# Kernel optimization log

Hardware: AMD Instinct MI355X
Metric: run time of the kernel (lower is better)

Reference implementation:

```python
import jax, jax.numpy as jnp
import numpy as np

B, G, P, E, H, K = 16, 512, 512, 256, 16, 16
CLIP = 10.0

def setup_inputs() -> dict:
    key = jax.random.key(0)
    ks = jax.random.split(key, 10)
    d = {
        "input1": jax.random.normal(ks[0], (B, 1, E), jnp.float32),
        "input2": jax.random.normal(ks[1], (B, G, E), jnp.float32),
        "current_time": jax.random.uniform(ks[2], (B, G, 1), jnp.float32),
        "ninf_mask": jnp.zeros((B, G, P), jnp.float32),
        "encoded_nodes": jax.random.normal(ks[3], (B, P, E), jnp.float32),
        # learned params (Linear weights stored [in, out]; y = x @ W)
        "Wq": jax.random.normal(ks[4], (2 * E + 1, H * K), jnp.float32) / np.sqrt(2 * E + 1),
        "Wk": jax.random.normal(ks[5], (E, H * K), jnp.float32) / np.sqrt(E),
        "Wv": jax.random.normal(ks[6], (E, H * K), jnp.float32) / np.sqrt(E),
        "Wc_w": jax.random.normal(ks[7], (H * K, E), jnp.float32) / np.sqrt(H * K),
        "Wc_b": jax.random.normal(ks[8], (E,), jnp.float32) * 0.01,
    }
    return d

def _heads(x):  # [B, N, H*K] -> [B, H, N, K]
    b, n, _ = x.shape
    return x.reshape(b, n, H, K).transpose(0, 2, 1, 3)

def reference(input1, input2, current_time, ninf_mask, encoded_nodes, Wq, Wk, Wv, Wc_w, Wc_b):
    # reset(): precompute k, v, single_head_key from encoded_nodes
    k = _heads(encoded_nodes @ Wk)  # [B,H,P,K]
    v = _heads(encoded_nodes @ Wv)  # [B,H,P,K]

    # forward()
    input_cat = jnp.concatenate(
        (jnp.broadcast_to(input1, (B, G, E)), input2, current_time), axis=2)  # [B,G,2E+1]
    q = _heads(input_cat @ Wq)  # [B,H,G,K]

    # MHA with additive ninf mask
    score = jnp.einsum("bhgk,bhpk->bhgp", q, k) / np.sqrt(K)
    score = score + ninf_mask[:, None, :, :]
    weights = jax.nn.softmax(score, axis=3)
    out = jnp.einsum("bhgp,bhpk->bhgk", weights, v)
    out_concat = out.transpose(0, 2, 1, 3).reshape(B, G, H * K)
    mh_atten_out = out_concat @ Wc_w + Wc_b  # [B,G,E]

    # single-head pointer score with tanh clipping
    score2 = jnp.einsum("bge,bpe->bgp", mh_atten_out, encoded_nodes) / np.sqrt(E)
    score_clipped = CLIP * jnp.tanh(score2)
    probs = jax.nn.softmax(score_clipped + ninf_mask, axis=2)
    return probs
```

## Files before the change

kernel.cpp:

```cpp
#include <hip/hip_runtime.h>
#include <math.h>

#define BB 16
#define GG 512
#define PP 512
#define EE 256
#define HH 16
#define KD 16
#define HK 256

typedef __bf16 bf16x8 __attribute__((ext_vector_type(8)));
typedef __bf16 bf16x4 __attribute__((ext_vector_type(4)));
typedef float f32x4 __attribute__((ext_vector_type(4)));
typedef float f32x16 __attribute__((ext_vector_type(16)));

#define SA_STRIDE 40
#define SMEM_BYTES 30720

__device__ inline void cvt_split8(const float* __restrict__ p, bf16x8& h, bf16x8& l)
{
    float4 f0 = *(const float4*)p;
    float4 f1 = *(const float4*)(p + 4);
    float v[8] = {f0.x, f0.y, f0.z, f0.w, f1.x, f1.y, f1.z, f1.w};
#pragma unroll
    for (int j = 0; j < 8; ++j) {
        __bf16 hh = (__bf16)v[j];
        h[j] = hh;
        l[j] = (__bf16)(v[j] - (float)hh);
    }
}

__global__ __launch_bounds__(256) void weight_prep(const float* __restrict__ Wk,
                                                   const float* __restrict__ Wv,
                                                   const float* __restrict__ Wq,
                                                   const float* __restrict__ Wc,
                                                   __bf16* __restrict__ wkt_h, __bf16* __restrict__ wkt_l,
                                                   __bf16* __restrict__ wvt_h, __bf16* __restrict__ wvt_l,
                                                   __bf16* __restrict__ wqt_h, __bf16* __restrict__ wqt_l,
                                                   __bf16* __restrict__ wct_h, __bf16* __restrict__ wct_l)
{
    int id = blockIdx.x * 256 + threadIdx.x;
    const float* W;
    __bf16 *th, *tl;
    int kbits;
    if (id < 65536)       { W = Wk; th = wkt_h; tl = wkt_l; kbits = 8; }
    else if (id < 131072) { id -= 65536;  W = Wv; th = wvt_h; tl = wvt_l; kbits = 8; }
    else if (id < 262144) { id -= 131072; W = Wq; th = wqt_h; tl = wqt_l; kbits = 9; }
    else                  { id -= 262144; W = Wc; th = wct_h; tl = wct_l; kbits = 8; }
    const int Kd = 1 << kbits;
    const int k = id & (Kd - 1);
    const int n = id >> kbits;
    const float v = W[(size_t)k * HK + n];
    const __bf16 h = (__bf16)v;
    th[((size_t)n << kbits) + k] = h;
    tl[((size_t)n << kbits) + k] = (__bf16)(v - (float)h);
}

__device__ inline void kvproj_body(int bx, int tid, unsigned char* smem,
                                   const float* __restrict__ A,
                                   const __bf16* __restrict__ Bkh,
                                   const __bf16* __restrict__ Bkl,
                                   const __bf16* __restrict__ Bvh,
                                   const __bf16* __restrict__ Bvl,
                                   __bf16* __restrict__ Khi,
                                   __bf16* __restrict__ Klo,
                                   __bf16* __restrict__ Vt)
{
    __bf16* sAh = (__bf16*)smem;
    __bf16* sAl = sAh + 64 * SA_STRIDE;
    __bf16* sB  = sAl + 64 * SA_STRIDE;

    const int lane = tid & 63;
    const int w = __builtin_amdgcn_readfirstlane(tid >> 6);
    const int m0 = (bx >> 2) * 64;
    const int n0 = (bx & 3) * 64;
    const int wm = (w >> 1) * 32, wn = (w & 1) * 32;
    const int ln = lane & 15, kq = (lane >> 4) * 8;
    const int ar = tid >> 2, ac = (tid & 3) * 8;

    const __bf16* bsel = (w == 0) ? Bkh : (w == 1) ? Bkl : (w == 2) ? Bvh : Bvl;

    f32x4 ak[2][2], av[2][2];
#pragma unroll
    for (int i = 0; i < 2; ++i)
#pragma unroll
        for (int j = 0; j < 2; ++j) {
            ak[i][j] = (f32x4){0.f, 0.f, 0.f, 0.f};
            av[i][j] = (f32x4){0.f, 0.f, 0.f, 0.f};
        }

    for (int k0 = 0; k0 < EE; k0 += 32) {
        {
            bf16x8 h8, l8;
            cvt_split8(A + (size_t)(m0 + ar) * EE + k0 + ac, h8, l8);
            *(bf16x8*)&sAh[ar * SA_STRIDE + ac] = h8;
            *(bf16x8*)&sAl[ar * SA_STRIDE + ac] = l8;
        }
        {
            const __bf16* src = bsel + (size_t)(n0 + lane) * EE + k0;
            __bf16* dst = sB + (w * 64 + lane) * SA_STRIDE;
            *(bf16x8*)&dst[0]  = *(const bf16x8*)&src[0];
            *(bf16x8*)&dst[8]  = *(const bf16x8*)&src[8];
            *(bf16x8*)&dst[16] = *(const bf16x8*)&src[16];
            *(bf16x8*)&dst[24] = *(const bf16x8*)&src[24];
        }
        __syncthreads();

        bf16x8 ah[2], al[2];
#pragma unroll
        for (int mt = 0; mt < 2; ++mt) {
            ah[mt] = *(const bf16x8*)&sAh[(wm + mt * 16 + ln) * SA_STRIDE + kq];
            al[mt] = *(const bf16x8*)&sAl[(wm + mt * 16 + ln) * SA_STRIDE + kq];
        }
#pragma unroll
        for (int nt = 0; nt < 2; ++nt) {
            const int rowb = wn + nt * 16 + ln;
            bf16x8 bkh8 = *(const bf16x8*)&sB[(0 * 64 + rowb) * SA_STRIDE + kq];
            bf16x8 bkl8 = *(const bf16x8*)&sB[(1 * 64 + rowb) * SA_STRIDE + kq];
            bf16x8 bvh8 = *(const bf16x8*)&sB[(2 * 64 + rowb) * SA_STRIDE + kq];
            bf16x8 bvl8 = *(const bf16x8*)&sB[(3 * 64 + rowb) * SA_STRIDE + kq];
#pragma unroll
            for (int mt = 0; mt < 2; ++mt) {
                ak[mt][nt] = __builtin_amdgcn_mfma_f32_16x16x32_bf16(ah[mt], bkh8, ak[mt][nt], 0, 0, 0);
                ak[mt][nt] = __builtin_amdgcn_mfma_f32_16x16x32_bf16(al[mt], bkh8, ak[mt][nt], 0, 0, 0);
                ak[mt][nt] = __builtin_amdgcn_mfma_f32_16x16x32_bf16(ah[mt], bkl8, ak[mt][nt], 0, 0, 0);
                av[mt][nt] = __builtin_amdgcn_mfma_f32_16x16x32_bf16(ah[mt], bvh8, av[mt][nt], 0, 0, 0);
                av[mt][nt] = __builtin_amdgcn_mfma_f32_16x16x32_bf16(al[mt], bvh8, av[mt][nt], 0, 0, 0);
                av[mt][nt] = __builtin_amdgcn_mfma_f32_16x16x32_bf16(ah[mt], bvl8, av[mt][nt], 0, 0, 0);
            }
        }
        __syncthreads();
    }

    __bf16* eKh = (__bf16*)smem;
    __bf16* eKl = eKh + 5120;
    __bf16* eV  = eKl + 5120;

    const int rbase = (lane >> 4) * 4;
#pragma unroll
    for (int mt = 0; mt < 2; ++mt)
#pragma unroll
        for (int nt = 0; nt < 2; ++nt) {
            const int hloc = (w & 1) * 2 + nt;
            const int nl = wn + nt * 16 + ln;
#pragma unroll
            for (int r = 0; r < 4; ++r) {
                const int m = wm + mt * 16 + rbase + r;
                const float vk = ak[mt][nt][r];
                const __bf16 hk = (__bf16)vk;
                eKh[(hloc * 64 + m) * 20 + ln] = hk;
                eKl[(hloc * 64 + m) * 20 + ln] = (__bf16)(vk - (float)hk);
                eV[nl * 68 + m] = (__bf16)av[mt][nt][r];
            }
        }
    __syncthreads();

    const int b = m0 >> 9;
    const int pbase = m0 & (PP - 1);
    {
        const int hl = tid >> 6, p = tid & 63;
        const int hg = (n0 >> 4) + hl;
        const size_t dst = (((size_t)b * HH + hg) * PP + pbase + p) * KD;
        const int base = (hl * 64 + p) * 20;
        uint2 a0 = *(const uint2*)&eKh[base + 0];
        uint2 a1 = *(const uint2*)&eKh[base + 4];
        uint2 a2 = *(const uint2*)&eKh[base + 8];
        uint2 a3 = *(const uint2*)&eKh[base + 12];
        *(uint4*)(Khi + dst)     = make_uint4(a0.x, a0.y, a1.x, a1.y);
        *(uint4*)(Khi + dst + 8) = make_uint4(a2.x, a2.y, a3.x, a3.y);
        uint2 c0 = *(const uint2*)&eKl[base + 0];
        uint2 c1 = *(const uint2*)&eKl[base + 4];
        uint2 c2 = *(const uint2*)&eKl[base + 8];
        uint2 c3 = *(const uint2*)&eKl[base + 12];
        *(uint4*)(Klo + dst)     = make_uint4(c0.x, c0.y, c1.x, c1.y);
        *(uint4*)(Klo + dst + 8) = make_uint4(c2.x, c2.y, c3.x, c3.y);
    }
    {
        const int n = tid >> 2, qq = tid & 3;
        const int ng = n0 + n, hg = ng >> 4, kk = ng & 15;
        const int base = n * 68 + qq * 16;
        uint2 v0 = *(const uint2*)&eV[base + 0];
        uint2 v1 = *(const uint2*)&eV[base + 4];
        uint2 v2 = *(const uint2*)&eV[base + 8];
        uint2 v3 = *(const uint2*)&eV[base + 12];
        const size_t dst = ((((size_t)b * HH + hg) * KD + kk) * PP) + pbase + qq * 16;
        *(uint4*)(Vt + dst)     = make_uint4(v0.x, v0.y, v1.x, v1.y);
        *(uint4*)(Vt + dst + 8) = make_uint4(v2.x, v2.y, v3.x, v3.y);
    }
}

__device__ inline void qproj_body(int bx, int tid, unsigned char* smem,
                                  const float* __restrict__ in1,
                                  const float* __restrict__ in2,
                                  const float* __restrict__ ct,
                                  const __bf16* __restrict__ Bh,
                                  const __bf16* __restrict__ Bl,
                                  const float* __restrict__ WqFull,
                                  __bf16* __restrict__ Qhi,
                                  __bf16* __restrict__ Qlo)
{
    __bf16* sAh = (__bf16*)smem;
    __bf16* sAl = sAh + 64 * SA_STRIDE;
    __bf16* sB  = sAl + 64 * SA_STRIDE;

    const int lane = tid & 63;
    const int w = __builtin_amdgcn_readfirstlane(tid >> 6);
    const int m0 = (bx >> 2) * 64;
    const int n0 = (bx & 3) * 64;
    const int wm = (w >> 1) * 32, wn = (w & 1) * 32;
    const int ln = lane & 15, kq = (lane >> 4) * 8;
    const int ar = tid >> 2, ac = (tid & 3) * 8;
    const int b = m0 >> 9;
    const float* WqLast = WqFull + (size_t)512 * HK;

    f32x4 acc[2][2];
#pragma unroll
    for (int i = 0; i < 2; ++i)
#pragma unroll
        for (int j = 0; j < 2; ++j) acc[i][j] = (f32x4){0.f, 0.f, 0.f, 0.f};

    for (int k0 = 0; k0 < 512; k0 += 32) {
        {
            const float* ap = (k0 < 256)
                ? in1 + (size_t)b * EE + k0 + ac
                : in2 + (size_t)(m0 + ar) * EE + (k0 - 256) + ac;
            bf16x8 h8, l8;
            cvt_split8(ap, h8, l8);
            *(bf16x8*)&sAh[ar * SA_STRIDE + ac] = h8;
            *(bf16x8*)&sAl[ar * SA_STRIDE + ac] = l8;
        }
        {
            const int mat = w >> 1;
            const int row = (w & 1) * 32 + (lane >> 1);
            const int half = (lane & 1) * 16;
            const __bf16* src = (mat ? Bl : Bh) + ((size_t)(n0 + row) << 9) + k0 + half;
            __bf16* dst = sB + (mat * 64 + row) * SA_STRIDE + half;
            *(bf16x8*)&dst[0] = *(const bf16x8*)&src[0];
            *(bf16x8*)&dst[8] = *(const bf16x8*)&src[8];
        }
        __syncthreads();

        bf16x8 ah[2], al[2];
#pragma unroll
        for (int mt = 0; mt < 2; ++mt) {
            ah[mt] = *(const bf16x8*)&sAh[(wm + mt * 16 + ln) * SA_STRIDE + kq];
            al[mt] = *(const bf16x8*)&sAl[(wm + mt * 16 + ln) * SA_STRIDE + kq];
        }
#pragma unroll
        for (int nt = 0; nt < 2; ++nt) {
            const int rowb = wn + nt * 16 + ln;
            bf16x8 bh8 = *(const bf16x8*)&sB[(0 * 64 + rowb) * SA_STRIDE + kq];
            bf16x8 bl8 = *(const bf16x8*)&sB[(1 * 64 + rowb) * SA_STRIDE + kq];
#pragma unroll
            for (int mt = 0; mt < 2; ++mt) {
                acc[mt][nt] = __builtin_amdgcn_mfma_f32_16x16x32_bf16(ah[mt], bh8, acc[mt][nt], 0, 0, 0);
                acc[mt][nt] = __builtin_amdgcn_mfma_f32_16x16x32_bf16(al[mt], bh8, acc[mt][nt], 0, 0, 0);
                acc[mt][nt] = __builtin_amdgcn_mfma_f32_16x16x32_bf16(ah[mt], bl8, acc[mt][nt], 0, 0, 0);
            }
        }
        __syncthreads();
    }

    __bf16* eQh = (__bf16*)smem;
    __bf16* eQl = eQh + 5120;

    const int rbase = (lane >> 4) * 4;
#pragma unroll
    for (int mt = 0; mt < 2; ++mt)
#pragma unroll
        for (int nt = 0; nt < 2; ++nt) {
            const int hloc = (w & 1) * 2 + nt;
            const int ng = n0 + wn + nt * 16 + ln;
            const float wq = WqLast[ng];
#pragma unroll
            for (int r = 0; r < 4; ++r) {
                const int m = wm + mt * 16 + rbase + r;
                const float v = acc[mt][nt][r] + ct[m0 + m] * wq;
                const __bf16 h = (__bf16)v;
                eQh[(hloc * 64 + m) * 20 + ln] = h;
                eQl[(hloc * 64 + m) * 20 + ln] = (__bf16)(v - (float)h);
            }
        }
    __syncthreads();

    {
        const int hl = tid >> 6, p = tid & 63;
        const int hg = (n0 >> 4) + hl;
        const int g = (m0 & (GG - 1)) + p;
        const size_t dst = (((size_t)b * HH + hg) * GG + g) * KD;
        const int base = (hl * 64 + p) * 20;
        uint2 a0 = *(const uint2*)&eQh[base + 0];
        uint2 a1 = *(const uint2*)&eQh[base + 4];
        uint2 a2 = *(const uint2*)&eQh[base + 8];
        uint2 a3 = *(const uint2*)&eQh[base + 12];
        *(uint4*)(Qhi + dst)     = make_uint4(a0.x, a0.y, a1.x, a1.y);
        *(uint4*)(Qhi + dst + 8) = make_uint4(a2.x, a2.y, a3.x, a3.y);
        uint2 c0 = *(const uint2*)&eQl[base + 0];
        uint2 c1 = *(const uint2*)&eQl[base + 4];
        uint2 c2 = *(const uint2*)&eQl[base + 8];
        uint2 c3 = *(const uint2*)&eQl[base + 12];
        *(uint4*)(Qlo + dst)     = make_uint4(c0.x, c0.y, c1.x, c1.y);
        *(uint4*)(Qlo + dst + 8) = make_uint4(c2.x, c2.y, c3.x, c3.y);
    }
}

__global__ __launch_bounds__(256, 2) void fused_proj(const float* __restrict__ enc,
                                                     const __bf16* __restrict__ Bkh,
                                                     const __bf16* __restrict__ Bkl,
                                                     const __bf16* __restrict__ Bvh,
                                                     const __bf16* __restrict__ Bvl,
                                                     __bf16* __restrict__ Khi,
                                                     __bf16* __restrict__ Klo,
                                                     __bf16* __restrict__ Vt,
                                                     const float* __restrict__ in1,
                                                     const float* __restrict__ in2,
                                                     const float* __restrict__ ct,
                                                     const __bf16* __restrict__ Bqh,
                                                     const __bf16* __restrict__ Bql,
                                                     const float* __restrict__ WqFull,
                                                     __bf16* __restrict__ Qhi,
                                                     __bf16* __restrict__ Qlo)
{
    __shared__ __align__(16) unsigned char smem[SMEM_BYTES];
    const int id = blockIdx.x;
    if (id < 512)
        kvproj_body(id, threadIdx.x, smem, enc, Bkh, Bkl, Bvh, Bvl, Khi, Klo, Vt);
    else
        qproj_body(id - 512, threadIdx.x, smem, in1, in2, ct, Bqh, Bql, WqFull, Qhi, Qlo);
}

__global__ __launch_bounds__(256, 4) void attn_v8(const __bf16* __restrict__ Qhi,
                                                  const __bf16* __restrict__ Qlo,
                                                  const __bf16* __restrict__ Khi,
                                                  const __bf16* __restrict__ Klo,
                                                  const __bf16* __restrict__ Vt,
                                                  const float* __restrict__ mask,
                                                  __bf16* __restrict__ Ath,
                                                  __bf16* __restrict__ Atl)
{
    __shared__ __align__(16) __bf16 sP[4][32][40];
    __shared__ float srs[4][32];

    const int t = threadIdx.x;
    const int lane = t & 63;
    const int w = __builtin_amdgcn_readfirstlane(t >> 6);
    const int g0 = blockIdx.x * 32;
    const int h = blockIdx.y * 4 + w;
    const int b = blockIdx.z;
    const int ln32 = lane & 31;
    const int half = lane >> 5;
    const int ln16 = lane & 15;
    const int quad = (lane >> 4) & 3;

    const size_t qbase = (((size_t)b * HH + h) * GG + g0) * KD;
    const size_t kbase = ((size_t)b * HH + h) * PP * KD;
    const size_t vbase = ((size_t)b * HH + h) * KD * PP;
    const float* mbase = mask + ((size_t)(b * GG + g0)) * PP;

    bf16x8 qah = *(const bf16x8*)(Qhi + qbase + (size_t)ln32 * KD + half * 8);
    bf16x8 qal = *(const bf16x8*)(Qlo + qbase + (size_t)ln32 * KD + half * 8);

    float rs[16];
#pragma unroll
    for (int r = 0; r < 16; ++r) rs[r] = 0.f;
    f32x4 o0 = (f32x4){0.f, 0.f, 0.f, 0.f};
    f32x4 o1 = (f32x4){0.f, 0.f, 0.f, 0.f};

#pragma unroll 2
    for (int pc = 0; pc < 16; ++pc) {
        const int pb = pc * 32;
        const size_t ko = kbase + (size_t)(pb + ln32) * KD + half * 8;
        bf16x8 kh = *(const bf16x8*)(Khi + ko);
        bf16x8 kl = *(const bf16x8*)(Klo + ko);

        f32x16 s = (f32x16){0.f, 0.f, 0.f, 0.f, 0.f, 0.f, 0.f, 0.f,
                            0.f, 0.f, 0.f, 0.f, 0.f, 0.f, 0.f, 0.f};
        s = __builtin_amdgcn_mfma_f32_32x32x16_bf16(qah, kh, s, 0, 0, 0);
        s = __builtin_amdgcn_mfma_f32_32x32x16_bf16(qal, kh, s, 0, 0, 0);
        s = __builtin_amdgcn_mfma_f32_32x32x16_bf16(qah, kl, s, 0, 0, 0);

#pragma unroll
        for (int r = 0; r < 16; ++r) {
            const int row = (r & 3) + 8 * (r >> 2) + 4 * half;
            const float m = mbase[(size_t)row * PP + pb + ln32];
            const float e = __expf(s[r] * 0.25f + m);
            rs[r] += e;
            sP[w][row][ln32] = (__bf16)e;
        }

        bf16x8 vb = *(const bf16x8*)(Vt + vbase + (size_t)ln16 * PP + pb + quad * 8);
        bf16x8 p0 = *(const bf16x8*)&sP[w][ln16][quad * 8];
        bf16x8 p1 = *(const bf16x8*)&sP[w][16 + ln16][quad * 8];
        o0 = __builtin_amdgcn_mfma_f32_16x16x32_bf16(p0, vb, o0, 0, 0, 0);
        o1 = __builtin_amdgcn_mfma_f32_16x16x32_bf16(p1, vb, o1, 0, 0, 0);
    }

#pragma unroll
    for (int r = 0; r < 16; ++r) {
#pragma unroll
        for (int mm = 1; mm < 32; mm <<= 1) rs[r] += __shfl_xor(rs[r], mm);
    }
    if (ln32 == 0) {
#pragma unroll
        for (int r = 0; r < 16; ++r)
            srs[w][(r & 3) + 8 * (r >> 2) + 4 * half] = rs[r];
    }

#pragma unroll
    for (int t2 = 0; t2 < 2; ++t2) {
        const f32x4 oc = t2 ? o1 : o0;
#pragma unroll
        for (int r = 0; r < 4; ++r) {
            const int grow = t2 * 16 + quad * 4 + r;
            const float v = oc[r] / srs[w][grow];
            const __bf16 hv = (__bf16)v;
            const size_t oo = ((size_t)(b * GG + g0 + grow)) * HK + h * KD + ln16;
            Ath[oo] = hv;
            Atl[oo] = (__bf16)(v - (float)hv);
        }
    }
}

__device__ inline void outproj_body(int bx, int tid,
                                    const __bf16* __restrict__ Ah,
                                    const __bf16* __restrict__ Al,
                                    const __bf16* __restrict__ Bh,
                                    const __bf16* __restrict__ Bl,
                                    const float* __restrict__ bias,
                                    __bf16* __restrict__ Ch,
                                    __bf16* __restrict__ Cl)
{
    const int lane = tid & 63, w = tid >> 6;
    const int m0 = (bx >> 2) * 64 + (w >> 1) * 32;
    const int n0 = (bx & 3) * 64 + (w & 1) * 32;
    const int ln = lane & 15, kc = (lane >> 4) * 8;

    f32x4 acc[2][2];
#pragma unroll
    for (int i = 0; i < 2; ++i)
#pragma unroll
        for (int j = 0; j < 2; ++j) acc[i][j] = (f32x4){0.f, 0.f, 0.f, 0.f};

    for (int k0 = 0; k0 < EE; k0 += 32) {
        bf16x8 ah[2], al[2], bh[2], bl[2];
#pragma unroll
        for (int mt = 0; mt < 2; ++mt) {
            const size_t o = (size_t)(m0 + mt * 16 + ln) * EE + k0 + kc;
            ah[mt] = *(const bf16x8*)(Ah + o);
            al[mt] = *(const bf16x8*)(Al + o);
        }
#pragma unroll
        for (int nt = 0; nt < 2; ++nt) {
            const size_t o = (size_t)(n0 + nt * 16 + ln) * EE + k0 + kc;
            bh[nt] = *(const bf16x8*)(Bh + o);
            bl[nt] = *(const bf16x8*)(Bl + o);
        }
#pragma unroll
        for (int mt = 0; mt < 2; ++mt)
#pragma unroll
            for (int nt = 0; nt < 2; ++nt) {
                acc[mt][nt] = __builtin_amdgcn_mfma_f32_16x16x32_bf16(ah[mt], bh[nt], acc[mt][nt], 0, 0, 0);
                acc[mt][nt] = __builtin_amdgcn_mfma_f32_16x16x32_bf16(al[mt], bh[nt], acc[mt][nt], 0, 0, 0);
                acc[mt][nt] = __builtin_amdgcn_mfma_f32_16x16x32_bf16(ah[mt], bl[nt], acc[mt][nt], 0, 0, 0);
            }
    }

    const int rbase = (lane >> 4) * 4;
#pragma unroll
    for (int mt = 0; mt < 2; ++mt)
#pragma unroll
        for (int nt = 0; nt < 2; ++nt)
#pragma unroll
            for (int r = 0; r < 4; ++r) {
                const int m = m0 + rbase + r + mt * 16;
                const int n = n0 + nt * 16 + ln;
                const float v = acc[mt][nt][r] + bias[n];
                const __bf16 h = (__bf16)v;
                Ch[(size_t)m * HK + n] = h;
                Cl[(size_t)m * HK + n] = (__bf16)(v - (float)h);
            }
}

__global__ __launch_bounds__(256) void fused_post(const __bf16* __restrict__ Ah,
                                                  const __bf16* __restrict__ Al,
                                                  const __bf16* __restrict__ Bh,
                                                  const __bf16* __restrict__ Bl,
                                                  const float* __restrict__ bias,
                                                  __bf16* __restrict__ Ch,
                                                  __bf16* __restrict__ Cl,
                                                  const float* __restrict__ enc,
                                                  __bf16* __restrict__ enc_h,
                                                  __bf16* __restrict__ enc_l)
{
    const int id = blockIdx.x;
    if (id < 512) {
        outproj_body(id, threadIdx.x, Ah, Al, Bh, Bl, bias, Ch, Cl);
    } else {
        const int i = ((id - 512) * 256 + threadIdx.x) * 4;
        float4 v = *(const float4*)(enc + i);
        bf16x4 h, l;
        h[0] = (__bf16)v.x; l[0] = (__bf16)(v.x - (float)h[0]);
        h[1] = (__bf16)v.y; l[1] = (__bf16)(v.y - (float)h[1]);
        h[2] = (__bf16)v.z; l[2] = (__bf16)(v.z - (float)h[2]);
        h[3] = (__bf16)v.w; l[3] = (__bf16)(v.w - (float)h[3]);
        *(bf16x4*)(enc_h + i) = h;
        *(bf16x4*)(enc_l + i) = l;
    }
}

__global__ __launch_bounds__(512) void pointer_v3(const __bf16* __restrict__ mh_hi,
                                                  const __bf16* __restrict__ mh_lo,
                                                  const __bf16* __restrict__ enc_hi,
                                                  const __bf16* __restrict__ enc_lo,
                                                  const float* __restrict__ mask,
                                                  float* __restrict__ out)
{
    __shared__ float swsum[8][32];
    const int t = threadIdx.x;
    const int lane = t & 63;
    const int w = __builtin_amdgcn_readfirstlane(t >> 6);
    const int id = blockIdx.x;
    const int b = id & 15;
    const int g0 = (id >> 4) * 32;
    const int ln32 = lane & 31;
    const int half = lane >> 5;

    const size_t arow = ((size_t)(b * GG + g0 + ln32)) * EE + half * 8;
    const size_t brow = ((size_t)(b * PP + w * 64 + ln32)) * EE + half * 8;

    f32x16 acc[2];
#pragma unroll
    for (int pt = 0; pt < 2; ++pt)
        acc[pt] = (f32x16){0.f, 0.f, 0.f, 0.f, 0.f, 0.f, 0.f, 0.f,
                           0.f, 0.f, 0.f, 0.f, 0.f, 0.f, 0.f, 0.f};

    for (int kc = 0; kc < EE; kc += 16) {
        bf16x8 ah = *(const bf16x8*)(mh_hi + arow + kc);
        bf16x8 al = *(const bf16x8*)(mh_lo + arow + kc);
#pragma unroll
        for (int pt = 0; pt < 2; ++pt) {
            const size_t bo = brow + (size_t)pt * 32 * EE + kc;
            bf16x8 bh = *(const bf16x8*)(enc_hi + bo);
            bf16x8 bl = *(const bf16x8*)(enc_lo + bo);
            acc[pt] = __builtin_amdgcn_mfma_f32_32x32x16_bf16(ah, bh, acc[pt], 0, 0, 0);
            acc[pt] = __builtin_amdgcn_mfma_f32_32x32x16_bf16(al, bh, acc[pt], 0, 0, 0);
            acc[pt] = __builtin_amdgcn_mfma_f32_32x32x16_bf16(ah, bl, acc[pt], 0, 0, 0);
        }
    }

    float rsum[16];
#pragma unroll
    for (int r = 0; r < 16; ++r) rsum[r] = 0.f;
#pragma unroll
    for (int pt = 0; pt < 2; ++pt)
#pragma unroll
        for (int r = 0; r < 16; ++r) {
            const int row = (r & 3) + 8 * (r >> 2) + 4 * half;
            float s = acc[pt][r] * 0.0625f;
            s = fminf(9.f, fmaxf(-9.f, s));
            const float e2 = __expf(2.f * s);
            const float th = (e2 - 1.f) / (e2 + 1.f);
            const float m = mask[((size_t)(b * GG + g0 + row)) * PP + w * 64 + pt * 32 + ln32];
            const float e = __expf(10.f * th + m);
            acc[pt][r] = e;
            rsum[r] += e;
        }

#pragma unroll
    for (int r = 0; r < 16; ++r) {
        rsum[r] += __shfl_xor(rsum[r], 1);
        rsum[r] += __shfl_xor(rsum[r], 2);
        rsum[r] += __shfl_xor(rsum[r], 4);
        rsum[r] += __shfl_xor(rsum[r], 8);
        rsum[r] += __shfl_xor(rsum[r], 16);
    }
    if (ln32 == 0) {
#pragma unroll
        for (int r = 0; r < 16; ++r)
            swsum[w][(r & 3) + 8 * (r >> 2) + 4 * half] = rsum[r];
    }
    __syncthreads();

    float inv[16];
#pragma unroll
    for (int r = 0; r < 16; ++r) {
        const int row = (r & 3) + 8 * (r >> 2) + 4 * half;
        float tot = 0.f;
#pragma unroll
        for (int wv = 0; wv < 8; ++wv) tot += swsum[wv][row];
        inv[r] = 1.f / tot;
    }

#pragma unroll
    for (int pt = 0; pt < 2; ++pt)
#pragma unroll
        for (int r = 0; r < 16; ++r) {
            const int row = (r & 3) + 8 * (r >> 2) + 4 * half;
            out[((size_t)(b * GG + g0 + row)) * PP + w * 64 + pt * 32 + ln32] =
                acc[pt][r] * inv[r];
        }
}

extern "C" void kernel_launch(void* const* d_in, const int* in_sizes, int n_in,
                              void* d_out, int out_size, void* d_ws, size_t ws_size,
                              hipStream_t stream)
{
    const float* in1  = (const float*)d_in[0];
    const float* in2  = (const float*)d_in[1];
    const float* ct   = (const float*)d_in[2];
    const float* mask = (const float*)d_in[3];
    const float* enc  = (const float*)d_in[4];
    const float* Wq   = (const float*)d_in[5];
    const float* Wk   = (const float*)d_in[6];
    const float* Wv   = (const float*)d_in[7];
    const float* Wcw  = (const float*)d_in[8];
    const float* Wcb  = (const float*)d_in[9];
    float* out = (float*)d_out;
    float* ws  = (float*)d_ws;

    const size_t SEG = (size_t)BB * GG * HK;
    __bf16* Khi = (__bf16*)ws;
    __bf16* Klo = Khi + SEG;
    __bf16* Vt  = (__bf16*)(ws + SEG);
    __bf16* Ath = Vt + SEG;
    __bf16* Qhi = (__bf16*)(ws + 2 * SEG);
    __bf16* Qlo = Qhi + SEG;
    __bf16* wkt_h = (__bf16*)(ws + 3 * SEG);
    __bf16* wkt_l = wkt_h + 65536;
    __bf16* wvt_h = wkt_l + 65536;
    __bf16* wvt_l = wvt_h + 65536;
    __bf16* wqt_h = wvt_l + 65536;
    __bf16* wqt_l = wqt_h + 131072;
    __bf16* wct_h = wqt_l + 131072;
    __bf16* wct_l = wct_h + 65536;
    __bf16* Atl   = (__bf16*)(ws + 3 * SEG) + 1048576;
    __bf16* mh_h  = (__bf16*)ws;
    __bf16* mh_l  = mh_h + SEG;
    __bf16* enc_h = (__bf16*)(ws + 2 * SEG);
    __bf16* enc_l = enc_h + SEG;

    const dim3 blk(256);

    weight_prep<<<dim3(1280), blk, 0, stream>>>(Wk, Wv, Wq, Wcw,
                                                wkt_h, wkt_l, wvt_h, wvt_l,
                                                wqt_h, wqt_l, wct_h, wct_l);

    fused_proj<<<dim3(1024), blk, 0, stream>>>(enc, wkt_h, wkt_l, wvt_h, wvt_l,
                                               Khi, Klo, Vt,
                                               in1, in2, ct, wqt_h, wqt_l, Wq,
                                               Qhi, Qlo);

    attn_v8<<<dim3(GG / 32, HH / 4, BB), blk, 0, stream>>>(Qhi, Qlo, Khi, Klo, Vt, mask, Ath, Atl);

    fused_post<<<dim3(2560), blk, 0, stream>>>(Ath, Atl, wct_h, wct_l, Wcb,
                                               mh_h, mh_l, enc, enc_h, enc_l);

    pointer_v3<<<dim3(256), dim3(512), 0, stream>>>(mh_h, mh_l, enc_h, enc_l, mask, out);
}
```

Before: 204.0 us.

## Fuse output projection into pointer kernel and emit enc split from KV projection

Removes the separate fused_post launch. The output projection (attention out @ Wc + bias) now runs inside the pointer kernel, with each 512-thread block computing its 32x256 mh tile into shared memory before the pointer-score MFMA loop. The enc hi/lo bf16 split is now written by the KV projection blocks that already convert enc (only the n0==0 column tile). Workspace buffers get disjoint slots so they no longer alias. The pointer kernel gains LDS use and a serial projection phase on only 256 blocks, which may lower parallelism for that stage.

```diff
diff --git a/kernel.cpp b/kernel.cpp
--- a/kernel.cpp
+++ b/kernel.cpp
@@ -64,7 +64,9 @@
                                    const __bf16* __restrict__ Bvl,
                                    __bf16* __restrict__ Khi,
                                    __bf16* __restrict__ Klo,
-                                   __bf16* __restrict__ Vt)
+                                   __bf16* __restrict__ Vt,
+                                   __bf16* __restrict__ enc_h,
+                                   __bf16* __restrict__ enc_l)
 {
     __bf16* sAh = (__bf16*)smem;
     __bf16* sAl = sAh + 64 * SA_STRIDE;
@@ -95,6 +97,11 @@
             cvt_split8(A + (size_t)(m0 + ar) * EE + k0 + ac, h8, l8);
             *(bf16x8*)&sAh[ar * SA_STRIDE + ac] = h8;
             *(bf16x8*)&sAl[ar * SA_STRIDE + ac] = l8;
+            if (n0 == 0) {
+                const size_t eo = (size_t)(m0 + ar) * EE + k0 + ac;
+                *(bf16x8*)(enc_h + eo) = h8;
+                *(bf16x8*)(enc_l + eo) = l8;
+            }
         }
         {
             const __bf16* src = bsel + (size_t)(n0 + lane) * EE + k0;
@@ -312,6 +319,8 @@
                                                      __bf16* __restrict__ Khi,
                                                      __bf16* __restrict__ Klo,
                                                      __bf16* __restrict__ Vt,
+                                                     __bf16* __restrict__ enc_h,
+                                                     __bf16* __restrict__ enc_l,
                                                      const float* __restrict__ in1,
                                                      const float* __restrict__ in2,
                                                      const float* __restrict__ ct,
@@ -324,7 +333,7 @@
     __shared__ __align__(16) unsigned char smem[SMEM_BYTES];
     const int id = blockIdx.x;
     if (id < 512)
-        kvproj_body(id, threadIdx.x, smem, enc, Bkh, Bkl, Bvh, Bvl, Khi, Klo, Vt);
+        kvproj_body(id, threadIdx.x, smem, enc, Bkh, Bkl, Bvh, Bvl, Khi, Klo, Vt, enc_h, enc_l);
     else
         qproj_body(id - 512, threadIdx.x, smem, in1, in2, ct, Bqh, Bql, WqFull, Qhi, Qlo);
 }
@@ -421,101 +430,20 @@
     }
 }
 
-__device__ inline void outproj_body(int bx, int tid,
-                                    const __bf16* __restrict__ Ah,
-                                    const __bf16* __restrict__ Al,
-                                    const __bf16* __restrict__ Bh,
-                                    const __bf16* __restrict__ Bl,
-                                    const float* __restrict__ bias,
-                                    __bf16* __restrict__ Ch,
-                                    __bf16* __restrict__ Cl)
-{
-    const int lane = tid & 63, w = tid >> 6;
-    const int m0 = (bx >> 2) * 64 + (w >> 1) * 32;
-    const int n0 = (bx & 3) * 64 + (w & 1) * 32;
-    const int ln = lane & 15, kc = (lane >> 4) * 8;
-
-    f32x4 acc[2][2];
-#pragma unroll
-    for (int i = 0; i < 2; ++i)
-#pragma unroll
-        for (int j = 0; j < 2; ++j) acc[i][j] = (f32x4){0.f, 0.f, 0.f, 0.f};
-
-    for (int k0 = 0; k0 < EE; k0 += 32) {
-        bf16x8 ah[2], al[2], bh[2], bl[2];
-#pragma unroll
-        for (int mt = 0; mt < 2; ++mt) {
-            const size_t o = (size_t)(m0 + mt * 16 + ln) * EE + k0 + kc;
-            ah[mt] = *(const bf16x8*)(Ah + o);
-            al[mt] = *(const bf16x8*)(Al + o);
-        }
-#pragma unroll
-        for (int nt = 0; nt < 2; ++nt) {
-            const size_t o = (size_t)(n0 + nt * 16 + ln) * EE + k0 + kc;
-            bh[nt] = *(const bf16x8*)(Bh + o);
-            bl[nt] = *(const bf16x8*)(Bl + o);
-        }
-#pragma unroll
-        for (int mt = 0; mt < 2; ++mt)
-#pragma unroll
-            for (int nt = 0; nt < 2; ++nt) {
-                acc[mt][nt] = __builtin_amdgcn_mfma_f32_16x16x32_bf16(ah[mt], bh[nt], acc[mt][nt], 0, 0, 0);
-                acc[mt][nt] = __builtin_amdgcn_mfma_f32_16x16x32_bf16(al[mt], bh[nt], acc[mt][nt], 0, 0, 0);
-                acc[mt][nt] = __builtin_amdgcn_mfma_f32_16x16x32_bf16(ah[mt], bl[nt], acc[mt][nt], 0, 0, 0);
-            }
-    }
-
-    const int rbase = (lane >> 4) * 4;
-#pragma unroll
-    for (int mt = 0; mt < 2; ++mt)
-#pragma unroll
-        for (int nt = 0; nt < 2; ++nt)
-#pragma unroll
-            for (int r = 0; r < 4; ++r) {
-                const int m = m0 + rbase + r + mt * 16;
-                const int n = n0 + nt * 16 + ln;
-                const float v = acc[mt][nt][r] + bias[n];
-                const __bf16 h = (__bf16)v;
-                Ch[(size_t)m * HK + n] = h;
-                Cl[(size_t)m * HK + n] = (__bf16)(v - (float)h);
-            }
-}
-
-__global__ __launch_bounds__(256) void fused_post(const __bf16* __restrict__ Ah,
-                                                  const __bf16* __restrict__ Al,
-                                                  const __bf16* __restrict__ Bh,
-                                                  const __bf16* __restrict__ Bl,
+__global__ __launch_bounds__(512) void pointer_v4(const __bf16* __restrict__ Ath,
+                                                  const __bf16* __restrict__ Atl,
+                                                  const __bf16* __restrict__ wct_h,
+                                                  const __bf16* __restrict__ wct_l,
                                                   const float* __restrict__ bias,
-                                                  __bf16* __restrict__ Ch,
-                                                  __bf16* __restrict__ Cl,
-                                                  const float* __restrict__ enc,
-                                                  __bf16* __restrict__ enc_h,
-                                                  __bf16* __restrict__ enc_l)
-{
-    const int id = blockIdx.x;
-    if (id < 512) {
-        outproj_body(id, threadIdx.x, Ah, Al, Bh, Bl, bias, Ch, Cl);
-    } else {
-        const int i = ((id - 512) * 256 + threadIdx.x) * 4;
-        float4 v = *(const float4*)(enc + i);
-        bf16x4 h, l;
-        h[0] = (__bf16)v.x; l[0] = (__bf16)(v.x - (float)h[0]);
-        h[1] = (__bf16)v.y; l[1] = (__bf16)(v.y - (float)h[1]);
-        h[2] = (__bf16)v.z; l[2] = (__bf16)(v.z - (float)h[2]);
-        h[3] = (__bf16)v.w; l[3] = (__bf16)(v.w - (float)h[3]);
-        *(bf16x4*)(enc_h + i) = h;
-        *(bf16x4*)(enc_l + i) = l;
-    }
-}
-
-__global__ __launch_bounds__(512) void pointer_v3(const __bf16* __restrict__ mh_hi,
-                                                  const __bf16* __restrict__ mh_lo,
                                                   const __bf16* __restrict__ enc_hi,
                                                   const __bf16* __restrict__ enc_lo,
                                                   const float* __restrict__ mask,
                                                   float* __restrict__ out)
 {
+    __shared__ __align__(16) __bf16 smh_h[32][264];
+    __shared__ __align__(16) __bf16 smh_l[32][264];
     __shared__ float swsum[8][32];
+
     const int t = threadIdx.x;
     const int lane = t & 63;
     const int w = __builtin_amdgcn_readfirstlane(t >> 6);
@@ -525,7 +453,34 @@
     const int ln32 = lane & 31;
     const int half = lane >> 5;
 
-    const size_t arow = ((size_t)(b * GG + g0 + ln32)) * EE + half * 8;
+    {
+        const int n0w = w * 32;
+        const size_t aarow = ((size_t)(b * GG + g0 + ln32)) * HK + half * 8;
+        const size_t wrow  = ((size_t)(n0w + ln32)) * EE + half * 8;
+
+        f32x16 macc = (f32x16){0.f, 0.f, 0.f, 0.f, 0.f, 0.f, 0.f, 0.f,
+                               0.f, 0.f, 0.f, 0.f, 0.f, 0.f, 0.f, 0.f};
+        for (int kc = 0; kc < EE; kc += 16) {
+            bf16x8 ah = *(const bf16x8*)(Ath + aarow + kc);
+            bf16x8 al = *(const bf16x8*)(Atl + aarow + kc);
+            bf16x8 bh = *(const bf16x8*)(wct_h + wrow + kc);
+            bf16x8 bl = *(const bf16x8*)(wct_l + wrow + kc);
+            macc = __builtin_amdgcn_mfma_f32_32x32x16_bf16(ah, bh, macc, 0, 0, 0);
+            macc = __builtin_amdgcn_mfma_f32_32x32x16_bf16(al, bh, macc, 0, 0, 0);
+            macc = __builtin_amdgcn_mfma_f32_32x32x16_bf16(ah, bl, macc, 0, 0, 0);
+        }
+        const float bs = bias[n0w + ln32];
+#pragma unroll
+        for (int r = 0; r < 16; ++r) {
+            const int row = (r & 3) + 8 * (r >> 2) + 4 * half;
+            const float v = macc[r] + bs;
+            const __bf16 h = (__bf16)v;
+            smh_h[row][n0w + ln32] = h;
+            smh_l[row][n0w + ln32] = (__bf16)(v - (float)h);
+        }
+    }
+    __syncthreads();
+
     const size_t brow = ((size_t)(b * PP + w * 64 + ln32)) * EE + half * 8;
 
     f32x16 acc[2];
@@ -535,8 +490,8 @@
                            0.f, 0.f, 0.f, 0.f, 0.f, 0.f, 0.f, 0.f};
 
     for (int kc = 0; kc < EE; kc += 16) {
-        bf16x8 ah = *(const bf16x8*)(mh_hi + arow + kc);
-        bf16x8 al = *(const bf16x8*)(mh_lo + arow + kc);
+        bf16x8 ah = *(const bf16x8*)&smh_h[ln32][kc + half * 8];
+        bf16x8 al = *(const bf16x8*)&smh_l[ln32][kc + half * 8];
 #pragma unroll
         for (int pt = 0; pt < 2; ++pt) {
             const size_t bo = brow + (size_t)pt * 32 * EE + kc;
@@ -616,16 +571,19 @@
     const float* Wcw  = (const float*)d_in[8];
     const float* Wcb  = (const float*)d_in[9];
     float* out = (float*)d_out;
-    float* ws  = (float*)d_ws;
 
     const size_t SEG = (size_t)BB * GG * HK;
-    __bf16* Khi = (__bf16*)ws;
-    __bf16* Klo = Khi + SEG;
-    __bf16* Vt  = (__bf16*)(ws + SEG);
-    __bf16* Ath = Vt + SEG;
-    __bf16* Qhi = (__bf16*)(ws + 2 * SEG);
-    __bf16* Qlo = Qhi + SEG;
-    __bf16* wkt_h = (__bf16*)(ws + 3 * SEG);
+    __bf16* base = (__bf16*)d_ws;
+    __bf16* Khi   = base + 0 * SEG;
+    __bf16* Klo   = base + 1 * SEG;
+    __bf16* Vt    = base + 2 * SEG;
+    __bf16* Qhi   = base + 3 * SEG;
+    __bf16* Qlo   = base + 4 * SEG;
+    __bf16* Ath   = base + 5 * SEG;
+    __bf16* Atl   = base + 6 * SEG;
+    __bf16* enc_h = base + 7 * SEG;
+    __bf16* enc_l = base + 8 * SEG;
+    __bf16* wkt_h = base + 9 * SEG;
     __bf16* wkt_l = wkt_h + 65536;
     __bf16* wvt_h = wkt_l + 65536;
     __bf16* wvt_l = wvt_h + 65536;
@@ -633,11 +591,6 @@
     __bf16* wqt_l = wqt_h + 131072;
     __bf16* wct_h = wqt_l + 131072;
     __bf16* wct_l = wct_h + 65536;
-    __bf16* Atl   = (__bf16*)(ws + 3 * SEG) + 1048576;
-    __bf16* mh_h  = (__bf16*)ws;
-    __bf16* mh_l  = mh_h + SEG;
-    __bf16* enc_h = (__bf16*)(ws + 2 * SEG);
-    __bf16* enc_l = enc_h + SEG;
 
     const dim3 blk(256);
 
@@ -646,14 +599,12 @@
                                                 wqt_h, wqt_l, wct_h, wct_l);
 
     fused_proj<<<dim3(1024), blk, 0, stream>>>(enc, wkt_h, wkt_l, wvt_h, wvt_l,
-                                               Khi, Klo, Vt,
+                                               Khi, Klo, Vt, enc_h, enc_l,
                                                in1, in2, ct, wqt_h, wqt_l, Wq,
                                                Qhi, Qlo);
 
     attn_v8<<<dim3(GG / 32, HH / 4, BB), blk, 0, stream>>>(Qhi, Qlo, Khi, Klo, Vt, mask, Ath, Atl);
 
-    fused_post<<<dim3(2560), blk, 0, stream>>>(Ath, Atl, wct_h, wct_l, Wcb,
-                                               mh_h, mh_l, enc, enc_h, enc_l);
-
-    pointer_v3<<<dim3(256), dim3(512), 0, stream>>>(mh_h, mh_l, enc_h, enc_l, mask, out);
-}
+    pointer_v4<<<dim3(256), dim3(512), 0, stream>>>(Ath, Atl, wct_h, wct_l, Wcb,
+                                                    enc_h, enc_l, mask, out);
+}
```

Result: no change. 204.3 us (+0.1%).
